# Kernel optimization log

Measured on AMD Instinct MI355X. Metric: run time of the kernel, lower is better.

The kernel has to match this reference:

```python
import jax, jax.numpy as jnp
import numpy as np

KS = 3          # image feature patch kernel size
RATE = 2        # downsample rate; alpha patches use kernel RATE*2, stride RATE
PENALTY = -10000.0
EPS = 1e-4
BN_EPS = 1e-5


def _pad(x, k, s):
    # reflect 'same' padding as in GCAModule.pad
    l = (k - s + 1) // 2
    r = (k - s) // 2
    return jnp.pad(x, ((0, 0), (0, 0), (l, r), (l, r)), mode='reflect')


def _extract_patches(x, k, s):
    # replicates reflect-pad + F.unfold + reshape -> (n, L, c, k, k)
    x = _pad(x, k, s)
    n, c, H, W = x.shape
    oh = (H - k) // s + 1
    ow = (W - k) // s + 1
    cols = [x[:, :, di:di + s * (oh - 1) + 1:s, dj:dj + s * (ow - 1) + 1:s]
            for di in range(k) for dj in range(k)]
    p = jnp.stack(cols, axis=2).reshape(n, c, k, k, oh * ow)  # (n,c,k,k,L)
    return jnp.transpose(p, (0, 4, 1, 2, 3))                  # (n,L,c,k,k)


def _deconv(score, kern):
    # torch: F.conv_transpose2d(score[None], kern, stride=RATE, padding=1) / 4
    # score: (L,h,w); kern: (L, ac, 4, 4) in torch conv_transpose (I,O,kh,kw) layout
    k = jnp.transpose(jnp.flip(kern, axis=(2, 3)), (1, 0, 2, 3))  # -> OIHW
    out = jax.lax.conv_general_dilated(
        score[None], k, window_strides=(1, 1), padding=[(2, 2), (2, 2)],
        lhs_dilation=(RATE, RATE), dimension_numbers=('NCHW', 'OIHW', 'NCHW'))
    return out[0] / 4.0


def gca_forward(img_feat, alpha_feat, unknown, gconv_w, gconv_b, oconv_w,
                bn_gamma, bn_beta):
    n = img_feat.shape[0]
    # guidance 1x1 conv + nearest downsample by RATE
    g = jnp.einsum('nchw,oc->nohw', img_feat, gconv_w) + gconv_b[None, :, None, None]
    g = g[:, :, ::RATE, ::RATE]
    u = unknown[:, :, ::RATE, ::RATE]
    # process_unknown_mask: per-sample softmax scales
    um = u.mean(axis=(2, 3))                                    # (n,1)
    km = 1.0 - um
    unknown_scale = jnp.clip(jnp.sqrt(um / km), 0.1, 10.0)      # (n,1)
    known_scale = jnp.clip(jnp.sqrt(km / um), 0.1, 10.0)        # (n,1)
    h, w = g.shape[2], g.shape[3]
    L = h * w
    img_ps = _extract_patches(g, KS, 1)                         # (n,L,c,3,3)
    alpha_ps = _extract_patches(alpha_feat, RATE * 2, RATE)     # (n,L,ac,4,4)
    unk_ps = _extract_patches(u, KS, 1)[:, :, 0].mean(axis=(2, 3))  # (n,L)
    # l2-normalized image patch kernels
    norm = jnp.sqrt(jnp.sum(img_ps * img_ps, axis=(2, 3, 4), keepdims=True))
    img_ps_n = img_ps / jnp.maximum(norm, EPS)
    # similarity: conv of padded g with patch kernels == patches-at-p . kernel-q
    sim = jnp.einsum('npckl,nqckl->nqp', img_ps, img_ps_n)      # (n,L,L)
    is_unknown = (unk_ps > 0.0).astype(sim.dtype)               # (n,L)
    scale = unknown_scale * is_unknown + known_scale * (1.0 - is_unknown)
    out = sim * scale[:, :, None]
    idx = jnp.arange(L)
    out = out.at[:, idx, idx].add(PENALTY * unk_ps)             # self-corr penalty
    gca = jax.nn.softmax(out, axis=1).reshape(n, L, h, w)
    prop = jax.vmap(_deconv)(gca, alpha_ps)                     # (n,ac,2h,2w)
    # out_conv: 1x1 conv (no bias) + BatchNorm (training stats) + residual
    y = jnp.einsum('nchw,oc->nohw', prop, oconv_w)
    mu = y.mean(axis=(0, 2, 3), keepdims=True)
    var = y.var(axis=(0, 2, 3), keepdims=True)
    y = (y - mu) / jnp.sqrt(var + BN_EPS)
    y = y * bn_gamma[None, :, None, None] + bn_beta[None, :, None, None]
    return y + alpha_feat


def setup_inputs():
    key = jax.random.key(0)
    ks = jax.random.split(key, 8)
    N, C, AC, H, W = 4, 256, 128, 64, 64
    img_feat = jax.random.normal(ks[0], (N, C, H, W), jnp.float32)
    alpha_feat = jax.random.normal(ks[1], (N, AC, H, W), jnp.float32)
    unknown = jax.random.randint(ks[2], (N, 1, H, W), 0, 2).astype(jnp.float32)
    gconv_w = jax.random.normal(ks[3], (C // 2, C), jnp.float32) / np.float32(np.sqrt(C))
    gconv_b = jax.random.normal(ks[4], (C // 2,), jnp.float32) * 0.01
    oconv_w = jax.random.normal(ks[5], (AC, AC), jnp.float32) / np.float32(np.sqrt(AC))
    bn_gamma = 0.001 + jax.random.normal(ks[6], (AC,), jnp.float32) * 0.001
    bn_beta = jax.random.normal(ks[7], (AC,), jnp.float32) * 0.001
    return dict(img_feat=img_feat, alpha_feat=alpha_feat, unknown=unknown,
                gconv_w=gconv_w, gconv_b=gconv_b, oconv_w=oconv_w,
                bn_gamma=bn_gamma, bn_beta=bn_beta)


def reference(img_feat, alpha_feat, unknown, gconv_w, gconv_b, oconv_w,
              bn_gamma, bn_beta):
    return gca_forward(img_feat, alpha_feat, unknown, gconv_w, gconv_b,
                       oconv_w, bn_gamma, bn_beta)
```

## Files before the change

kernel.cpp:

```cpp
#include <hip/hip_runtime.h>

#define NN 4
#define CIN 256
#define CH 128
#define HH 64
#define hh 32
#define L 1024
#define NB 2048
#define PENALTY -10000.0f
#define EPS 1e-4f

typedef __bf16 bf16x8 __attribute__((ext_vector_type(8)));
typedef float f32x4 __attribute__((ext_vector_type(4)));
typedef __attribute__((address_space(3))) void lds_t;
typedef __attribute__((address_space(1))) const void gbl_t;

__device__ __forceinline__ int refl32(int t) { return t < 0 ? -t : (t > 31 ? 62 - t : t); }
__device__ __forceinline__ int refl64(int t) { return t < 0 ? -t : (t > 63 ? 126 - t : t); }
__device__ __forceinline__ int swz(int k, int row) { return k ^ (((row >> 1) & 3) << 3); }

__global__ void k_prep(const float* __restrict__ img, const float* __restrict__ gw,
                       const float* __restrict__ ow, const float* __restrict__ unknown,
                       __bf16* __restrict__ Xb, __bf16* __restrict__ gwb,
                       __bf16* __restrict__ owb, float* __restrict__ unk,
                       float* __restrict__ scales) {
    __shared__ float sm[CIN * 33];
    int bid = blockIdx.x, t = threadIdx.x;
    if (bid < 128) {
        int i = bid & 31, n = bid >> 5;
        for (int e = t; e < CIN * 32; e += 256) {
            int c = e >> 5, jj = e & 31;
            sm[c * 33 + jj] = img[(((size_t)n * CIN + c) * HH + 2 * i) * HH + 2 * jj];
        }
        __syncthreads();
#pragma unroll
        for (int j = 0; j < 32; ++j) {
            int np = (n << 10) + i * 32 + j;
            int cl = swz(t, np);
            Xb[(size_t)np * CIN + t] = (__bf16)sm[cl * 33 + j];
        }
    } else if (bid < 132) {
        int n = bid - 128;
        float* u = sm;
        float* red = sm + 1024;
        float part = 0.f;
#pragma unroll
        for (int c = 0; c < 4; ++c) {
            int idx = t + c * 256;
            int i = idx >> 5, j = idx & 31;
            float v = unknown[n * 4096 + (2 * i) * HH + 2 * j];
            u[idx] = v;
            part += v;
        }
        red[t] = part;
        __syncthreads();
        for (int s = 128; s > 0; s >>= 1) {
            if (t < s) red[t] += red[t + s];
            __syncthreads();
        }
        if (t == 0) {
            float um = red[0] / 1024.0f;
            float km = 1.0f - um;
            scales[n * 2] = fminf(fmaxf(sqrtf(um / km), 0.1f), 10.0f);
            scales[n * 2 + 1] = fminf(fmaxf(sqrtf(km / um), 0.1f), 10.0f);
        }
#pragma unroll
        for (int c = 0; c < 4; ++c) {
            int idx = t + c * 256;
            int i = idx >> 5, j = idx & 31;
            float sum = 0.f;
#pragma unroll
            for (int di = -1; di <= 1; ++di)
#pragma unroll
                for (int dj = -1; dj <= 1; ++dj)
                    sum += u[refl32(i + di) * 32 + refl32(j + dj)];
            unk[n * L + idx] = sum * (1.0f / 9.0f);
        }
    } else {
        for (int e = (bid - 132) * 256 + t; e < 49152; e += 36 * 256) {
            if (e < 32768) {
                int o = e >> 8, m = e & 255;
                gwb[e] = (__bf16)gw[o * 256 + swz(m, o)];
            } else {
                int e2 = e - 32768;
                int j = e2 >> 7, m = e2 & 127;
                owb[e2] = (__bf16)ow[j * 128 + swz(m, j)];
            }
        }
    }
}

__global__ void k_btbuild(const float* __restrict__ alpha, __bf16* __restrict__ Bt) {
    __shared__ float sm[64 * 65];
    int blk = blockIdx.x;
    int n = blk >> 7, o = blk & 127;
    int t = threadIdx.x;
    const float* ap = alpha + ((size_t)(n * CH + o) << 12);
#pragma unroll
    for (int j = 0; j < 4; ++j) {
        int fi = t + j * 256;
        int row = fi >> 4, c4 = fi & 15;
        float4 v = *(const float4*)(ap + fi * 4);
        float* d = sm + row * 65 + c4 * 4;
        d[0] = v.x; d[1] = v.y; d[2] = v.z; d[3] = v.w;
    }
    __syncthreads();
    __bf16* Bn = Bt + ((size_t)(n * NB) << 10);
#pragma unroll
    for (int gi = 0; gi < 8; ++gi) {
        int g = gi * 256 + t;
        int ab = g >> 7, qg = g & 127;
        int a = ab >> 2, bb = ab & 3;
        int q0 = qg * 8;
        int qi = q0 >> 5, qj0 = q0 & 31;
        int ti = refl64(2 * qi + a - 1);
        const float* r = sm + ti * 65;
        __bf16 v[8];
#pragma unroll
        for (int s = 0; s < 8; ++s) v[s] = (__bf16)r[refl64(2 * (qj0 + s) + bb - 1)];
        int j = ab * 128 + o;
        *(bf16x8*)(Bn + ((size_t)j << 10) + swz(q0, j)) = *(bf16x8*)v;
    }
}

__global__ __launch_bounds__(256, 2) void k_gemm0(const __bf16* __restrict__ Xb,
                                                  const __bf16* __restrict__ gwb,
                                                  const float* __restrict__ gb,
                                                  __bf16* __restrict__ gbf) {
    __shared__ __align__(16) __bf16 As[128 * 32];
    __shared__ __align__(16) __bf16 Bs[128 * 32];
    int p0 = blockIdx.x * 128;
    int t = threadIdx.x, l = t & 63, w = t >> 6;
    int wr = w >> 1, wc = w & 1;
    f32x4 acc[4][4] = {};
    for (int k0 = 0; k0 < CIN; k0 += 32) {
#pragma unroll
        for (int i = 0; i < 2; ++i) {
            const __bf16* srcA = Xb + (size_t)(p0 + i * 64 + (t >> 2)) * CIN + k0 + (t & 3) * 8;
            __builtin_amdgcn_global_load_lds((gbl_t*)srcA, (lds_t*)(As + i * 2048 + t * 8), 16, 0, 0);
            const __bf16* srcB = gwb + (size_t)(i * 64 + (t >> 2)) * CIN + k0 + (t & 3) * 8;
            __builtin_amdgcn_global_load_lds((gbl_t*)srcB, (lds_t*)(Bs + i * 2048 + t * 8), 16, 0, 0);
        }
        __syncthreads();
        int gl = l >> 4, r = l & 15;
        bf16x8 av[4], bv[4];
#pragma unroll
        for (int m = 0; m < 4; ++m) {
            int row = wr * 64 + m * 16 + r;
            av[m] = *(const bf16x8*)(As + row * 32 + swz(gl << 3, row));
            int col = wc * 64 + m * 16 + r;
            bv[m] = *(const bf16x8*)(Bs + col * 32 + swz(gl << 3, col));
        }
#pragma unroll
        for (int m = 0; m < 4; ++m)
#pragma unroll
            for (int c2 = 0; c2 < 4; ++c2)
                acc[m][c2] = __builtin_amdgcn_mfma_f32_16x16x32_bf16(av[m], bv[c2], acc[m][c2], 0, 0, 0);
        __syncthreads();
    }
    int r = l & 15, hi = l >> 4;
#pragma unroll
    for (int m = 0; m < 4; ++m)
#pragma unroll
        for (int c2 = 0; c2 < 4; ++c2) {
            int o = wc * 64 + c2 * 16 + r;
            float bias = gb[o];
#pragma unroll
            for (int reg = 0; reg < 4; ++reg) {
                int row = p0 + wr * 64 + m * 16 + hi * 4 + reg;
                gbf[((size_t)row << 7) + o] = (__bf16)(acc[m][c2][reg] + bias);
            }
        }
}

__global__ void k_ssqf(const __bf16* __restrict__ gbf, const float* __restrict__ unk,
                       const float* __restrict__ scales, float* __restrict__ f) {
    __shared__ float ssqs[1024];
    int n = blockIdx.x, t = threadIdx.x;
#pragma unroll
    for (int c = 0; c < 4; ++c) {
        int row = t + c * 256;
        const __bf16* rp = gbf + (((size_t)(n << 10) + row) << 7);
        float s = 0.f;
#pragma unroll
        for (int kk = 0; kk < 16; ++kk) {
            bf16x8 v = *(const bf16x8*)(rp + kk * 8);
#pragma unroll
            for (int u2 = 0; u2 < 8; ++u2) {
                float x = (float)v[u2];
                s += x * x;
            }
        }
        ssqs[row] = s;
    }
    __syncthreads();
    float us = scales[n * 2], ks = scales[n * 2 + 1];
#pragma unroll
    for (int c = 0; c < 4; ++c) {
        int p = t + c * 256;
        int pi = p >> 5, pj = p & 31;
        float sum = 0.f;
#pragma unroll
        for (int di = -1; di <= 1; ++di)
#pragma unroll
            for (int dj = -1; dj <= 1; ++dj)
                sum += ssqs[refl32(pi + di) * 32 + refl32(pj + dj)];
        float norm = sqrtf(sum);
        float sc = unk[n * L + p] > 0.f ? us : ks;
        f[n * L + p] = sc / fmaxf(norm, EPS);
    }
}

__global__ __launch_bounds__(256, 1) void k_gemm1(const __bf16* __restrict__ gbf,
                                                  const float* __restrict__ f,
                                                  const float* __restrict__ unk,
                                                  float* __restrict__ W) {
    __shared__ __align__(16) __bf16 As[4 * 6144];
    __shared__ __align__(16) __bf16 Bs[4 * 6144];
    int n = blockIdx.z;
    int p0 = blockIdx.y * 128, q0 = blockIdx.x * 128;
    const __bf16* gn = gbf + ((size_t)n << 17);
    int t = threadIdx.x, l = t & 63, w = t >> 6;
    int wr = w >> 1, wc = w & 1;
    int by4 = blockIdx.y * 4, bx4 = blockIdx.x * 4;
    int rbA = by4 - 1; rbA = rbA < 0 ? 0 : (rbA > 26 ? 26 : rbA);
    int rbB = bx4 - 1; rbB = rbB < 0 ? 0 : (rbB > 26 ? 26 : rbB);
#pragma unroll
    for (int k = 0; k < 12; ++k) {
        int chunk = k / 3;
        int rem = (k % 3) * 256 + t;
        int wrow = rem >> 2, sg = rem & 3;
        int so = (chunk << 5) + ((sg ^ ((wrow >> 1) & 3)) << 3);
        int grA = ((rbA + (wrow >> 5)) << 5) + (wrow & 31);
        __builtin_amdgcn_global_load_lds((gbl_t*)(gn + (size_t)grA * 128 + so),
                                         (lds_t*)(As + chunk * 6144 + rem * 8), 16, 0, 0);
        int grB = ((rbB + (wrow >> 5)) << 5) + (wrow & 31);
        __builtin_amdgcn_global_load_lds((gbl_t*)(gn + (size_t)grB * 128 + so),
                                         (lds_t*)(Bs + chunk * 6144 + rem * 8), 16, 0, 0);
    }
    __syncthreads();
    int gl = l >> 4, r = l & 15;
    int rpA[4][3], cpA[4][3], rpB[4][3], cpB[4][3];
#pragma unroll
    for (int m = 0; m < 4; ++m) {
        int prow = wr * 64 + m * 16 + r;
        int qrow = wc * 64 + m * 16 + r;
#pragma unroll
        for (int d = 0; d < 3; ++d) {
            rpA[m][d] = (refl32(by4 + (prow >> 5) + d - 1) - rbA) << 10;
            int cp = refl32((prow & 31) + d - 1);
            cpA[m][d] = cp * 32 + ((gl ^ ((cp >> 1) & 3)) << 3);
            rpB[m][d] = (refl32(bx4 + (qrow >> 5) + d - 1) - rbB) << 10;
            int cq = refl32((qrow & 31) + d - 1);
            cpB[m][d] = cq * 32 + ((gl ^ ((cq >> 1) & 3)) << 3);
        }
    }
    f32x4 acc[4][4] = {};
#pragma unroll
    for (int dk = 0; dk < 3; ++dk)
#pragma unroll
        for (int dl = 0; dl < 3; ++dl)
#pragma unroll
            for (int cc = 0; cc < 4; ++cc) {
                bf16x8 av[4], bv[4];
#pragma unroll
                for (int m = 0; m < 4; ++m) {
                    av[m] = *(const bf16x8*)(As + cc * 6144 + rpA[m][dk] + cpA[m][dl]);
                    bv[m] = *(const bf16x8*)(Bs + cc * 6144 + rpB[m][dk] + cpB[m][dl]);
                }
#pragma unroll
                for (int m = 0; m < 4; ++m)
#pragma unroll
                    for (int c2 = 0; c2 < 4; ++c2)
                        acc[m][c2] = __builtin_amdgcn_mfma_f32_16x16x32_bf16(av[m], bv[c2], acc[m][c2], 0, 0, 0);
            }
    int hi = l >> 4;
#pragma unroll
    for (int m = 0; m < 4; ++m)
#pragma unroll
        for (int c2 = 0; c2 < 4; ++c2) {
            int q = q0 + wc * 64 + c2 * 16 + r;
            float fq = f[n * L + q];
#pragma unroll
            for (int reg = 0; reg < 4; ++reg) {
                int p = p0 + wr * 64 + m * 16 + hi * 4 + reg;
                float val = acc[m][c2][reg] * fq;
                if (p == q) val += PENALTY * unk[n * L + p];
                W[((size_t)n << 20) + ((size_t)p << 10) + q] = val;
            }
        }
}

__global__ void k_softmax(const float* __restrict__ W, __bf16* __restrict__ Wb) {
    __shared__ float red[8];
    int row = blockIdx.x;
    int p = row & (L - 1);
    const float* Wr = W + (size_t)row * 1024;
    __bf16* Wbr = Wb + (size_t)row * 1024;
    int t = threadIdx.x, wv = t >> 6;
    float v[4];
    float mx = -1e30f;
#pragma unroll
    for (int ll = 0; ll < 4; ++ll) {
        v[ll] = Wr[t + ll * 256];
        mx = fmaxf(mx, v[ll]);
    }
#pragma unroll
    for (int off = 32; off > 0; off >>= 1) mx = fmaxf(mx, __shfl_xor(mx, off));
    if ((t & 63) == 0) red[wv] = mx;
    __syncthreads();
    mx = fmaxf(fmaxf(red[0], red[1]), fmaxf(red[2], red[3]));
    float sum = 0.f;
#pragma unroll
    for (int ll = 0; ll < 4; ++ll) {
        v[ll] = __expf(v[ll] - mx);
        sum += v[ll];
    }
#pragma unroll
    for (int off = 32; off > 0; off >>= 1) sum += __shfl_xor(sum, off);
    if ((t & 63) == 0) red[4 + wv] = sum;
    __syncthreads();
    float inv = 1.0f / (red[4] + red[5] + red[6] + red[7]);
#pragma unroll
    for (int ll = 0; ll < 4; ++ll) Wbr[swz(t + ll * 256, p)] = (__bf16)(v[ll] * inv);
}

__global__ __launch_bounds__(256, 2) void k_gemm2(const __bf16* __restrict__ Wb,
                                                  const __bf16* __restrict__ Bt,
                                                  __bf16* __restrict__ Tb) {
    int bid = blockIdx.x;
    int xcd = bid & 7, idx = bid >> 3;
    int n = xcd >> 1;
    int p0 = ((xcd & 1) * 4 + (idx & 3)) * 128;
    int j0 = (idx >> 2) * 128;
    __shared__ __align__(16) __bf16 As[4][4096];
    __shared__ __align__(16) __bf16 Bs[4][4096];
    const __bf16* An = Wb + ((size_t)n << 20);
    const __bf16* Bn = Bt + ((size_t)n * NB << 10);
    int t = threadIdx.x, l = t & 63, w = t >> 6;
    int wr = w >> 1, wc = w & 1;
    int gl = l >> 4, r = l & 15;
    f32x4 acc[4][4] = {};

    auto stage = [&](int buf, int k0) {
#pragma unroll
        for (int i = 0; i < 2; ++i) {
            int row = (t >> 2) + i * 64;
            int sgo = (t & 3) * 8;
            const __bf16* srcA = An + ((size_t)(p0 + row) << 10) + k0 + sgo;
            __builtin_amdgcn_global_load_lds((gbl_t*)srcA, (lds_t*)(&As[buf][row * 32 + sgo]), 16, 0, 0);
            const __bf16* srcB = Bn + ((size_t)(j0 + row) << 10) + k0 + sgo;
            __builtin_amdgcn_global_load_lds((gbl_t*)srcB, (lds_t*)(&Bs[buf][row * 32 + sgo]), 16, 0, 0);
        }
    };
    auto compute = [&](int buf) {
        bf16x8 av[4], bv[4];
#pragma unroll
        for (int m = 0; m < 4; ++m) {
            int row = wr * 64 + m * 16 + r;
            av[m] = *(const bf16x8*)(&As[buf][row * 32 + ((gl ^ ((row >> 1) & 3)) << 3)]);
            int col = wc * 64 + m * 16 + r;
            bv[m] = *(const bf16x8*)(&Bs[buf][col * 32 + ((gl ^ ((col >> 1) & 3)) << 3)]);
        }
#pragma unroll
        for (int m = 0; m < 4; ++m)
#pragma unroll
            for (int c2 = 0; c2 < 4; ++c2)
                acc[m][c2] = __builtin_amdgcn_mfma_f32_16x16x32_bf16(av[m], bv[c2], acc[m][c2], 0, 0, 0);
    };

    stage(0, 0);
    stage(1, 32);
    for (int it = 0; it < 32; ++it) {
        int buf = it & 3;
        if (it + 2 < 32) stage((it + 2) & 3, (it + 2) * 32);
        if (it < 30)
            asm volatile("s_waitcnt vmcnt(8)\n\ts_barrier" ::: "memory");
        else if (it == 30)
            asm volatile("s_waitcnt vmcnt(4)\n\ts_barrier" ::: "memory");
        else
            asm volatile("s_waitcnt vmcnt(0)\n\ts_barrier" ::: "memory");
        compute(buf);
    }
    int hi = l >> 4;
#pragma unroll
    for (int m = 0; m < 4; ++m)
#pragma unroll
        for (int c2 = 0; c2 < 4; ++c2) {
            int j = j0 + wc * 64 + c2 * 16 + r;
#pragma unroll
            for (int reg = 0; reg < 4; ++reg) {
                int p = p0 + wr * 64 + m * 16 + hi * 4 + reg;
                Tb[((size_t)n * L + p) * NB + j] = (__bf16)acc[m][c2][reg];
            }
        }
}

__global__ void k_gather(const __bf16* __restrict__ Tb, __bf16* __restrict__ prop) {
    int e = blockIdx.x * 256 + threadIdx.x;
    int og = e & 15;
    int pix = (e >> 4) & 4095;
    int n = e >> 16;
    int x = pix & 63, y = pix >> 6;
    float acc[8] = {};
    int ap = (y + 1) & 1, bp = (x + 1) & 1;
    const __bf16* Tn = Tb + ((size_t)(n * L) << 11);
#pragma unroll
    for (int da = 0; da < 2; ++da) {
        int a = ap + 2 * da;
        int ny = y + 1 - a;
        if (ny < 0 || ny >= 64) continue;
        int py = ny >> 1;
#pragma unroll
        for (int db = 0; db < 2; ++db) {
            int bb = bp + 2 * db;
            int nx = x + 1 - bb;
            if (nx < 0 || nx >= 64) continue;
            int px = nx >> 1;
            bf16x8 v = *(const bf16x8*)(Tn + (((size_t)(py * hh + px)) << 11) + (a * 4 + bb) * 128 + og * 8);
#pragma unroll
            for (int u2 = 0; u2 < 8; ++u2) acc[u2] += (float)v[u2];
        }
    }
    __bf16 rr[8];
#pragma unroll
    for (int u2 = 0; u2 < 8; ++u2) rr[u2] = (__bf16)(acc[u2] * 0.25f);
    int dg = og ^ ((pix >> 1) & 3);
    *(bf16x8*)(prop + ((((size_t)(n << 12) + pix)) << 7) + dg * 8) = *(bf16x8*)rr;
}

__global__ __launch_bounds__(256, 2) void k_oconv(const __bf16* __restrict__ owb,
                                                  const __bf16* __restrict__ prop,
                                                  float* __restrict__ y2) {
    __shared__ __align__(16) __bf16 As[128 * 32];
    __shared__ __align__(16) __bf16 Bs[128 * 32];
    int n = blockIdx.z;
    int x0 = blockIdx.x * 128;
    const __bf16* Bn = prop + ((size_t)n << 19);
    int t = threadIdx.x, l = t & 63, w = t >> 6;
    int wr = w >> 1, wc = w & 1;
    f32x4 acc[4][4] = {};
    for (int k0 = 0; k0 < CH; k0 += 32) {
#pragma unroll
        for (int i = 0; i < 2; ++i) {
            const __bf16* srcA = owb + (size_t)(i * 64 + (t >> 2)) * CH + k0 + (t & 3) * 8;
            __builtin_amdgcn_global_load_lds((gbl_t*)srcA, (lds_t*)(As + i * 2048 + t * 8), 16, 0, 0);
            const __bf16* srcB = Bn + (size_t)(x0 + i * 64 + (t >> 2)) * CH + k0 + (t & 3) * 8;
            __builtin_amdgcn_global_load_lds((gbl_t*)srcB, (lds_t*)(Bs + i * 2048 + t * 8), 16, 0, 0);
        }
        __syncthreads();
        int gl = l >> 4, r = l & 15;
        bf16x8 av[4], bv[4];
#pragma unroll
        for (int m = 0; m < 4; ++m) {
            int row = wr * 64 + m * 16 + r;
            av[m] = *(const bf16x8*)(As + row * 32 + swz(gl << 3, row));
            int col = x0 + wc * 64 + m * 16 + r;
            bv[m] = *(const bf16x8*)(Bs + (wc * 64 + m * 16 + r) * 32 + swz(gl << 3, col));
        }
#pragma unroll
        for (int m = 0; m < 4; ++m)
#pragma unroll
            for (int c2 = 0; c2 < 4; ++c2)
                acc[m][c2] = __builtin_amdgcn_mfma_f32_16x16x32_bf16(av[m], bv[c2], acc[m][c2], 0, 0, 0);
        __syncthreads();
    }
    int r = l & 15, hi = l >> 4;
#pragma unroll
    for (int m = 0; m < 4; ++m)
#pragma unroll
        for (int c2 = 0; c2 < 4; ++c2) {
            int pix = x0 + wc * 64 + c2 * 16 + r;
#pragma unroll
            for (int reg = 0; reg < 4; ++reg) {
                int j = wr * 64 + m * 16 + hi * 4 + reg;
                y2[(((size_t)n * CH + j) << 12) + pix] = acc[m][c2][reg];
            }
        }
}

__global__ void k_bnstats(const float* __restrict__ y2, float* __restrict__ stats) {
    __shared__ float r1[256], r2[256];
    int oc = blockIdx.x, t = threadIdx.x;
    float s = 0.f, s2 = 0.f;
    for (int n = 0; n < NN; ++n) {
        const float* base = y2 + (((size_t)n * CH + oc) << 12);
        for (int pix = t; pix < 4096; pix += 256) {
            float v = base[pix];
            s += v;
            s2 += v * v;
        }
    }
    r1[t] = s;
    r2[t] = s2;
    __syncthreads();
    for (int st = 128; st > 0; st >>= 1) {
        if (t < st) {
            r1[t] += r1[t + st];
            r2[t] += r2[t + st];
        }
        __syncthreads();
    }
    if (t == 0) {
        stats[oc * 2] = r1[0];
        stats[oc * 2 + 1] = r2[0];
    }
}

__global__ void k_final(const float* __restrict__ y2, const float* __restrict__ stats,
                        const float* __restrict__ gamma, const float* __restrict__ beta,
                        const float* __restrict__ alpha, float* __restrict__ out) {
    int e = blockIdx.x * 256 + threadIdx.x;
    int oc = (e >> 12) & 127;
    float s1 = stats[oc * 2], s2 = stats[oc * 2 + 1];
    float mu = s1 * (1.0f / 16384.0f);
    float var = s2 * (1.0f / 16384.0f) - mu * mu;
    float inv = rsqrtf(var + 1e-5f);
    out[e] = (y2[e] - mu) * inv * gamma[oc] + beta[oc] + alpha[e];
}

extern "C" void kernel_launch(void* const* d_in, const int* in_sizes, int n_in,
                              void* d_out, int out_size, void* d_ws, size_t ws_size,
                              hipStream_t stream) {
    const float* img = (const float*)d_in[0];
    const float* alpha = (const float*)d_in[1];
    const float* unknown = (const float*)d_in[2];
    const float* gw = (const float*)d_in[3];
    const float* gb = (const float*)d_in[4];
    const float* ow = (const float*)d_in[5];
    const float* gamma = (const float*)d_in[6];
    const float* beta = (const float*)d_in[7];
    float* out = (float*)d_out;
    float* ws = (float*)d_ws;

    __bf16* Xb = (__bf16*)(ws);
    __bf16* gwb = (__bf16*)(ws + 524288);
    __bf16* owb = (__bf16*)(ws + 540672);
    __bf16* gbf = (__bf16*)(ws + 548864);
    float* f = ws + 811008;
    float* unk = ws + 815104;
    float* scales = ws + 819200;
    float* stats = ws + 819264;
    float* W = ws + 819520;
    __bf16* Wb = (__bf16*)(ws + 5013824);
    __bf16* Bt = (__bf16*)(ws + 7110976);
    __bf16* Tb = (__bf16*)(ws + 11305280);
    __bf16* prop = (__bf16*)(ws + 15499584);
    float* y2 = ws + 16548160;

    k_prep<<<168, 256, 0, stream>>>(img, gw, ow, unknown, Xb, gwb, owb, unk, scales);
    k_btbuild<<<512, 256, 0, stream>>>(alpha, Bt);
    k_gemm0<<<32, 256, 0, stream>>>(Xb, gwb, gb, gbf);
    k_ssqf<<<4, 256, 0, stream>>>(gbf, unk, scales, f);
    k_gemm1<<<dim3(8, 8, 4), 256, 0, stream>>>(gbf, f, unk, W);
    k_softmax<<<4096, 256, 0, stream>>>(W, Wb);
    k_gemm2<<<512, 256, 0, stream>>>(Wb, Bt, Tb);
    k_gather<<<1024, 256, 0, stream>>>(Tb, prop);
    k_oconv<<<dim3(32, 1, 4), 256, 0, stream>>>(owb, prop, y2);
    k_bnstats<<<128, 256, 0, stream>>>(y2, stats);
    k_final<<<8192, 256, 0, stream>>>(y2, stats, gamma, beta, alpha, out);
}
```

Baseline: 113.8 us.

## Fuse Bt build into prep, gather and BN stats into oconv, vectorize final

Merges the alpha patch-transpose kernel into the prep kernel, folds the deconvolution gather into the output 1x1-conv GEMM, and computes the batch-norm sums inside that GEMM with shuffles and atomics. This removes three launches and the bf16 prop round-trip through memory. The ssqf kernel now uses 1024 threads, and the final kernel uses float4 loads and stores. In exchange, the float atomics make the stats summation order nondeterministic, and the oconv tile shrinks to 64 pixels, so it launches twice as many blocks.

Result: faster. 102.7 us (-9.7%).

```diff
diff --git a/kernel.cpp b/kernel.cpp
--- a/kernel.cpp
+++ b/kernel.cpp
@@ -21,13 +21,44 @@
 
 __global__ void k_prep(const float* __restrict__ img, const float* __restrict__ gw,
                        const float* __restrict__ ow, const float* __restrict__ unknown,
+                       const float* __restrict__ alpha,
                        __bf16* __restrict__ Xb, __bf16* __restrict__ gwb,
                        __bf16* __restrict__ owb, float* __restrict__ unk,
-                       float* __restrict__ scales) {
+                       float* __restrict__ scales, __bf16* __restrict__ Bt,
+                       float* __restrict__ stats) {
     __shared__ float sm[CIN * 33];
     int bid = blockIdx.x, t = threadIdx.x;
-    if (bid < 128) {
-        int i = bid & 31, n = bid >> 5;
+    if (bid < 512) {
+        int n = bid >> 7, o = bid & 127;
+        const float* ap = alpha + ((size_t)(n * CH + o) << 12);
+#pragma unroll
+        for (int j = 0; j < 4; ++j) {
+            int fi = t + j * 256;
+            int row = fi >> 4, c4 = fi & 15;
+            float4 v = *(const float4*)(ap + fi * 4);
+            float* d = sm + row * 65 + c4 * 4;
+            d[0] = v.x; d[1] = v.y; d[2] = v.z; d[3] = v.w;
+        }
+        __syncthreads();
+        __bf16* Bn = Bt + ((size_t)(n * NB) << 10);
+#pragma unroll
+        for (int gi = 0; gi < 8; ++gi) {
+            int g = gi * 256 + t;
+            int ab = g >> 7, qg = g & 127;
+            int a = ab >> 2, bb = ab & 3;
+            int q0 = qg * 8;
+            int qi = q0 >> 5, qj0 = q0 & 31;
+            int ti = refl64(2 * qi + a - 1);
+            const float* r = sm + ti * 65;
+            __bf16 v[8];
+#pragma unroll
+            for (int s = 0; s < 8; ++s) v[s] = (__bf16)r[refl64(2 * (qj0 + s) + bb - 1)];
+            int j = ab * 128 + o;
+            *(bf16x8*)(Bn + ((size_t)j << 10) + swz(q0, j)) = *(bf16x8*)v;
+        }
+    } else if (bid < 640) {
+        int idx = bid - 512;
+        int i = idx & 31, n = idx >> 5;
         for (int e = t; e < CIN * 32; e += 256) {
             int c = e >> 5, jj = e & 31;
             sm[c * 33 + jj] = img[(((size_t)n * CIN + c) * HH + 2 * i) * HH + 2 * jj];
@@ -39,8 +70,8 @@
             int cl = swz(t, np);
             Xb[(size_t)np * CIN + t] = (__bf16)sm[cl * 33 + j];
         }
-    } else if (bid < 132) {
-        int n = bid - 128;
+    } else if (bid < 644) {
+        int n = bid - 640;
         float* u = sm;
         float* red = sm + 1024;
         float part = 0.f;
@@ -77,7 +108,8 @@
             unk[n * L + idx] = sum * (1.0f / 9.0f);
         }
     } else {
-        for (int e = (bid - 132) * 256 + t; e < 49152; e += 36 * 256) {
+        if (bid == 644) stats[t] = 0.f;
+        for (int e = (bid - 644) * 256 + t; e < 49152; e += 36 * 256) {
             if (e < 32768) {
                 int o = e >> 8, m = e & 255;
                 gwb[e] = (__bf16)gw[o * 256 + swz(m, o)];
@@ -87,39 +119,6 @@
                 owb[e2] = (__bf16)ow[j * 128 + swz(m, j)];
             }
         }
-    }
-}
-
-__global__ void k_btbuild(const float* __restrict__ alpha, __bf16* __restrict__ Bt) {
-    __shared__ float sm[64 * 65];
-    int blk = blockIdx.x;
-    int n = blk >> 7, o = blk & 127;
-    int t = threadIdx.x;
-    const float* ap = alpha + ((size_t)(n * CH + o) << 12);
-#pragma unroll
-    for (int j = 0; j < 4; ++j) {
-        int fi = t + j * 256;
-        int row = fi >> 4, c4 = fi & 15;
-        float4 v = *(const float4*)(ap + fi * 4);
-        float* d = sm + row * 65 + c4 * 4;
-        d[0] = v.x; d[1] = v.y; d[2] = v.z; d[3] = v.w;
-    }
-    __syncthreads();
-    __bf16* Bn = Bt + ((size_t)(n * NB) << 10);
-#pragma unroll
-    for (int gi = 0; gi < 8; ++gi) {
-        int g = gi * 256 + t;
-        int ab = g >> 7, qg = g & 127;
-        int a = ab >> 2, bb = ab & 3;
-        int q0 = qg * 8;
-        int qi = q0 >> 5, qj0 = q0 & 31;
-        int ti = refl64(2 * qi + a - 1);
-        const float* r = sm + ti * 65;
-        __bf16 v[8];
-#pragma unroll
-        for (int s = 0; s < 8; ++s) v[s] = (__bf16)r[refl64(2 * (qj0 + s) + bb - 1)];
-        int j = ab * 128 + o;
-        *(bf16x8*)(Bn + ((size_t)j << 10) + swz(q0, j)) = *(bf16x8*)v;
     }
 }
 
@@ -177,10 +176,8 @@
                        const float* __restrict__ scales, float* __restrict__ f) {
     __shared__ float ssqs[1024];
     int n = blockIdx.x, t = threadIdx.x;
-#pragma unroll
-    for (int c = 0; c < 4; ++c) {
-        int row = t + c * 256;
-        const __bf16* rp = gbf + (((size_t)(n << 10) + row) << 7);
+    {
+        const __bf16* rp = gbf + (((size_t)(n << 10) + t) << 7);
         float s = 0.f;
 #pragma unroll
         for (int kk = 0; kk < 16; ++kk) {
@@ -191,24 +188,20 @@
                 s += x * x;
             }
         }
-        ssqs[row] = s;
+        ssqs[t] = s;
     }
     __syncthreads();
     float us = scales[n * 2], ks = scales[n * 2 + 1];
-#pragma unroll
-    for (int c = 0; c < 4; ++c) {
-        int p = t + c * 256;
-        int pi = p >> 5, pj = p & 31;
-        float sum = 0.f;
-#pragma unroll
-        for (int di = -1; di <= 1; ++di)
-#pragma unroll
-            for (int dj = -1; dj <= 1; ++dj)
-                sum += ssqs[refl32(pi + di) * 32 + refl32(pj + dj)];
-        float norm = sqrtf(sum);
-        float sc = unk[n * L + p] > 0.f ? us : ks;
-        f[n * L + p] = sc / fmaxf(norm, EPS);
-    }
+    int pi = t >> 5, pj = t & 31;
+    float sum = 0.f;
+#pragma unroll
+    for (int di = -1; di <= 1; ++di)
+#pragma unroll
+        for (int dj = -1; dj <= 1; ++dj)
+            sum += ssqs[refl32(pi + di) * 32 + refl32(pj + dj)];
+    float norm = sqrtf(sum);
+    float sc = unk[n * L + t] > 0.f ? us : ks;
+    f[n * L + t] = sc / fmaxf(norm, EPS);
 }
 
 __global__ __launch_bounds__(256, 1) void k_gemm1(const __bf16* __restrict__ gbf,
@@ -396,127 +389,138 @@
         }
 }
 
-__global__ void k_gather(const __bf16* __restrict__ Tb, __bf16* __restrict__ prop) {
-    int e = blockIdx.x * 256 + threadIdx.x;
-    int og = e & 15;
-    int pix = (e >> 4) & 4095;
-    int n = e >> 16;
-    int x = pix & 63, y = pix >> 6;
-    float acc[8] = {};
-    int ap = (y + 1) & 1, bp = (x + 1) & 1;
-    const __bf16* Tn = Tb + ((size_t)(n * L) << 11);
-#pragma unroll
-    for (int da = 0; da < 2; ++da) {
-        int a = ap + 2 * da;
-        int ny = y + 1 - a;
-        if (ny < 0 || ny >= 64) continue;
-        int py = ny >> 1;
-#pragma unroll
-        for (int db = 0; db < 2; ++db) {
-            int bb = bp + 2 * db;
-            int nx = x + 1 - bb;
-            if (nx < 0 || nx >= 64) continue;
-            int px = nx >> 1;
-            bf16x8 v = *(const bf16x8*)(Tn + (((size_t)(py * hh + px)) << 11) + (a * 4 + bb) * 128 + og * 8);
-#pragma unroll
-            for (int u2 = 0; u2 < 8; ++u2) acc[u2] += (float)v[u2];
-        }
-    }
-    __bf16 rr[8];
-#pragma unroll
-    for (int u2 = 0; u2 < 8; ++u2) rr[u2] = (__bf16)(acc[u2] * 0.25f);
-    int dg = og ^ ((pix >> 1) & 3);
-    *(bf16x8*)(prop + ((((size_t)(n << 12) + pix)) << 7) + dg * 8) = *(bf16x8*)rr;
-}
-
-__global__ __launch_bounds__(256, 2) void k_oconv(const __bf16* __restrict__ owb,
-                                                  const __bf16* __restrict__ prop,
-                                                  float* __restrict__ y2) {
-    __shared__ __align__(16) __bf16 As[128 * 32];
-    __shared__ __align__(16) __bf16 Bs[128 * 32];
+__global__ void k_oconv(const __bf16* __restrict__ owb, const __bf16* __restrict__ Tb,
+                        float* __restrict__ y2, float* __restrict__ stats) {
+    __shared__ __align__(16) __bf16 As[4 * 4096];
+    __shared__ __align__(16) __bf16 Bp[4 * 2048];
     int n = blockIdx.z;
-    int x0 = blockIdx.x * 128;
-    const __bf16* Bn = prop + ((size_t)n << 19);
+    int x0 = blockIdx.x * 64;
     int t = threadIdx.x, l = t & 63, w = t >> 6;
     int wr = w >> 1, wc = w & 1;
-    f32x4 acc[4][4] = {};
-    for (int k0 = 0; k0 < CH; k0 += 32) {
+    int gl = l >> 4, r = l & 15, hi = l >> 4;
+#pragma unroll
+    for (int c = 0; c < 4; ++c)
 #pragma unroll
         for (int i = 0; i < 2; ++i) {
-            const __bf16* srcA = owb + (size_t)(i * 64 + (t >> 2)) * CH + k0 + (t & 3) * 8;
-            __builtin_amdgcn_global_load_lds((gbl_t*)srcA, (lds_t*)(As + i * 2048 + t * 8), 16, 0, 0);
-            const __bf16* srcB = Bn + (size_t)(x0 + i * 64 + (t >> 2)) * CH + k0 + (t & 3) * 8;
-            __builtin_amdgcn_global_load_lds((gbl_t*)srcB, (lds_t*)(Bs + i * 2048 + t * 8), 16, 0, 0);
-        }
-        __syncthreads();
-        int gl = l >> 4, r = l & 15;
-        bf16x8 av[4], bv[4];
+            int h = i * 256 + t;
+            const __bf16* src = owb + (size_t)(h >> 2) * CH + c * 32 + (h & 3) * 8;
+            __builtin_amdgcn_global_load_lds((gbl_t*)src, (lds_t*)(As + c * 4096 + h * 8), 16, 0, 0);
+        }
+    const __bf16* Tn = Tb + ((size_t)(n * L) << 11);
+#pragma unroll
+    for (int it = 0; it < 4; ++it) {
+        int e2 = it * 256 + t;
+        int og = e2 & 15, pl = e2 >> 4;
+        int pix = x0 + pl;
+        int x = pix & 63, y = pix >> 6;
+        float acc8[8] = {};
+        int ap = (y + 1) & 1, bp = (x + 1) & 1;
+#pragma unroll
+        for (int da = 0; da < 2; ++da) {
+            int a = ap + 2 * da;
+            int ny = y + 1 - a;
+            if (ny < 0 || ny >= 64) continue;
+            int py = ny >> 1;
+#pragma unroll
+            for (int db = 0; db < 2; ++db) {
+                int bb = bp + 2 * db;
+                int nx = x + 1 - bb;
+                if (nx < 0 || nx >= 64) continue;
+                int px = nx >> 1;
+                bf16x8 v = *(const bf16x8*)(Tn + (((size_t)(py * hh + px)) << 11) + (a * 4 + bb) * 128 + og * 8);
+#pragma unroll
+                for (int u2 = 0; u2 < 8; ++u2) acc8[u2] += (float)v[u2];
+            }
+        }
+        __bf16 rr[8];
+#pragma unroll
+        for (int u2 = 0; u2 < 8; ++u2) rr[u2] = (__bf16)(acc8[u2] * 0.25f);
+        int key = (pix >> 1) & 3;
+        int dgl = (og & 3) ^ key;
+        *(bf16x8*)(Bp + (og >> 2) * 2048 + pl * 32 + dgl * 8) = *(bf16x8*)rr;
+    }
+    __syncthreads();
+    f32x4 acc[4][2] = {};
+#pragma unroll
+    for (int c = 0; c < 4; ++c) {
+        bf16x8 av[4], bv[2];
 #pragma unroll
         for (int m = 0; m < 4; ++m) {
             int row = wr * 64 + m * 16 + r;
-            av[m] = *(const bf16x8*)(As + row * 32 + swz(gl << 3, row));
-            int col = x0 + wc * 64 + m * 16 + r;
-            bv[m] = *(const bf16x8*)(Bs + (wc * 64 + m * 16 + r) * 32 + swz(gl << 3, col));
+            av[m] = *(const bf16x8*)(As + c * 4096 + row * 32 + ((gl ^ ((row >> 1) & 3)) << 3));
+        }
+#pragma unroll
+        for (int c2 = 0; c2 < 2; ++c2) {
+            int col = wc * 32 + c2 * 16 + r;
+            bv[c2] = *(const bf16x8*)(Bp + c * 2048 + col * 32 + ((gl ^ ((col >> 1) & 3)) << 3));
         }
 #pragma unroll
         for (int m = 0; m < 4; ++m)
 #pragma unroll
-            for (int c2 = 0; c2 < 4; ++c2)
+            for (int c2 = 0; c2 < 2; ++c2)
                 acc[m][c2] = __builtin_amdgcn_mfma_f32_16x16x32_bf16(av[m], bv[c2], acc[m][c2], 0, 0, 0);
-        __syncthreads();
-    }
-    int r = l & 15, hi = l >> 4;
+    }
 #pragma unroll
     for (int m = 0; m < 4; ++m)
 #pragma unroll
-        for (int c2 = 0; c2 < 4; ++c2) {
-            int pix = x0 + wc * 64 + c2 * 16 + r;
+        for (int c2 = 0; c2 < 2; ++c2) {
+            int pix = x0 + wc * 32 + c2 * 16 + r;
 #pragma unroll
             for (int reg = 0; reg < 4; ++reg) {
                 int j = wr * 64 + m * 16 + hi * 4 + reg;
                 y2[(((size_t)n * CH + j) << 12) + pix] = acc[m][c2][reg];
             }
         }
-}
-
-__global__ void k_bnstats(const float* __restrict__ y2, float* __restrict__ stats) {
-    __shared__ float r1[256], r2[256];
-    int oc = blockIdx.x, t = threadIdx.x;
-    float s = 0.f, s2 = 0.f;
-    for (int n = 0; n < NN; ++n) {
-        const float* base = y2 + (((size_t)n * CH + oc) << 12);
-        for (int pix = t; pix < 4096; pix += 256) {
-            float v = base[pix];
-            s += v;
-            s2 += v * v;
-        }
-    }
-    r1[t] = s;
-    r2[t] = s2;
-    __syncthreads();
-    for (int st = 128; st > 0; st >>= 1) {
-        if (t < st) {
-            r1[t] += r1[t + st];
-            r2[t] += r2[t + st];
-        }
-        __syncthreads();
-    }
-    if (t == 0) {
-        stats[oc * 2] = r1[0];
-        stats[oc * 2 + 1] = r2[0];
+    __syncthreads();
+    float* partS = (float*)As;
+    float* partS2 = partS + 256;
+#pragma unroll
+    for (int m = 0; m < 4; ++m)
+#pragma unroll
+        for (int reg = 0; reg < 4; ++reg) {
+            float s = 0.f, s2 = 0.f;
+#pragma unroll
+            for (int c2 = 0; c2 < 2; ++c2) {
+                float v = acc[m][c2][reg];
+                s += v;
+                s2 += v * v;
+            }
+#pragma unroll
+            for (int off = 1; off < 16; off <<= 1) {
+                s += __shfl_xor(s, off);
+                s2 += __shfl_xor(s2, off);
+            }
+            if (r == 0) {
+                int j = wr * 64 + m * 16 + hi * 4 + reg;
+                partS[j * 2 + wc] = s;
+                partS2[j * 2 + wc] = s2;
+            }
+        }
+    __syncthreads();
+    if (t < 128) {
+        atomicAdd(&stats[t * 2], partS[t * 2] + partS[t * 2 + 1]);
+        atomicAdd(&stats[t * 2 + 1], partS2[t * 2] + partS2[t * 2 + 1]);
     }
 }
 
 __global__ void k_final(const float* __restrict__ y2, const float* __restrict__ stats,
                         const float* __restrict__ gamma, const float* __restrict__ beta,
                         const float* __restrict__ alpha, float* __restrict__ out) {
-    int e = blockIdx.x * 256 + threadIdx.x;
-    int oc = (e >> 12) & 127;
+    int e4 = blockIdx.x * 256 + threadIdx.x;
+    int oc = (e4 >> 10) & 127;
     float s1 = stats[oc * 2], s2 = stats[oc * 2 + 1];
     float mu = s1 * (1.0f / 16384.0f);
     float var = s2 * (1.0f / 16384.0f) - mu * mu;
     float inv = rsqrtf(var + 1e-5f);
-    out[e] = (y2[e] - mu) * inv * gamma[oc] + beta[oc] + alpha[e];
+    float g = gamma[oc], b = beta[oc];
+    float4 yv = ((const float4*)y2)[e4];
+    float4 av = ((const float4*)alpha)[e4];
+    float4 o;
+    o.x = (yv.x - mu) * inv * g + b + av.x;
+    o.y = (yv.y - mu) * inv * g + b + av.y;
+    o.z = (yv.z - mu) * inv * g + b + av.z;
+    o.w = (yv.w - mu) * inv * g + b + av.w;
+    ((float4*)out)[e4] = o;
 }
 
 extern "C" void kernel_launch(void* const* d_in, const int* in_sizes, int n_in,
@@ -545,18 +549,14 @@
     __bf16* Wb = (__bf16*)(ws + 5013824);
     __bf16* Bt = (__bf16*)(ws + 7110976);
     __bf16* Tb = (__bf16*)(ws + 11305280);
-    __bf16* prop = (__bf16*)(ws + 15499584);
-    float* y2 = ws + 16548160;
-
-    k_prep<<<168, 256, 0, stream>>>(img, gw, ow, unknown, Xb, gwb, owb, unk, scales);
-    k_btbuild<<<512, 256, 0, stream>>>(alpha, Bt);
+    float* y2 = ws + 15499584;
+
+    k_prep<<<680, 256, 0, stream>>>(img, gw, ow, unknown, alpha, Xb, gwb, owb, unk, scales, Bt, stats);
     k_gemm0<<<32, 256, 0, stream>>>(Xb, gwb, gb, gbf);
-    k_ssqf<<<4, 256, 0, stream>>>(gbf, unk, scales, f);
+    k_ssqf<<<4, 1024, 0, stream>>>(gbf, unk, scales, f);
     k_gemm1<<<dim3(8, 8, 4), 256, 0, stream>>>(gbf, f, unk, W);
     k_softmax<<<4096, 256, 0, stream>>>(W, Wb);
     k_gemm2<<<512, 256, 0, stream>>>(Wb, Bt, Tb);
-    k_gather<<<1024, 256, 0, stream>>>(Tb, prop);
-    k_oconv<<<dim3(32, 1, 4), 256, 0, stream>>>(owb, prop, y2);
-    k_bnstats<<<128, 256, 0, stream>>>(y2, stats);
-    k_final<<<8192, 256, 0, stream>>>(y2, stats, gamma, beta, alpha, out);
-}
+    k_oconv<<<dim3(64, 1, 4), 256, 0, stream>>>(owb, Tb, y2, stats);
+    k_final<<<2048, 256, 0, stream>>>(y2, stats, gamma, beta, alpha, out);
+}
```
